# Kernel tuning notes

Measured on AMD Instinct MI355X. Metric: run time of the kernel, lower is better.

Reference implementation:

```python
import jax, jax.numpy as jnp
import numpy as np

EMBED = 2048
HEADS = 16
NOPE = 128      # embed // heads
VDIM = 128
ROPE = 64
Q_HEAD = NOPE + ROPE  # 192
KV_RANK = 512
BASE = 10000.0


def _rope(x, offset=0):
    # x: [b, h, n, d] with d even; rotary (lrpe_type=1) on pair-interleaved dims
    d = x.shape[-1]
    n = x.shape[-2]
    theta = BASE ** (-2.0 * jnp.arange(d // 2, dtype=jnp.float32) / d)  # [d/2]
    pos = jnp.arange(n, dtype=jnp.float32) + offset                     # [n]
    ang = pos[:, None] * theta[None, :]                                  # [n, d/2]
    cos, sin = jnp.cos(ang), jnp.sin(ang)
    x1 = x[..., 0::2]
    x2 = x[..., 1::2]
    o1 = x1 * cos - x2 * sin
    o2 = x1 * sin + x2 * cos
    return jnp.stack([o1, o2], axis=-1).reshape(x.shape)


def setup_inputs() -> dict:
    key = jax.random.key(0)
    ks = jax.random.split(key, 6)
    b, n = 2, 2048
    s = lambda fin: 1.0 / np.sqrt(fin)
    return {
        "x": jax.random.normal(ks[0], (b, n, EMBED), jnp.float32),
        "Wqa": jax.random.normal(ks[1], (EMBED, 512), jnp.float32) * s(EMBED),
        "Wqb": jax.random.normal(ks[2], (512, HEADS * Q_HEAD), jnp.float32) * s(512),
        "Wkva": jax.random.normal(ks[3], (EMBED, KV_RANK + ROPE), jnp.float32) * s(EMBED),
        "Wkvb": jax.random.normal(ks[4], (KV_RANK, HEADS * (NOPE + VDIM)), jnp.float32) * s(KV_RANK),
        "Wout": jax.random.normal(ks[5], (HEADS * VDIM, EMBED), jnp.float32) * s(HEADS * VDIM),
    }


def reference(x, Wqa, Wqb, Wkva, Wkvb, Wout):
    b, n, _ = x.shape
    # low-rank Q projection
    q = (x @ Wqa) @ Wqb                                   # [b, n, h*192]
    q = q.reshape(b, n, HEADS, Q_HEAD).transpose(0, 2, 1, 3)  # [b, h, n, 192]
    q_nope, q_pe = q[..., :NOPE], q[..., NOPE:]
    # low-rank KV compression + shared rope key
    ckv = x @ Wkva                                        # [b, n, 512+64]
    compressed, k_pe = ckv[..., :KV_RANK], ckv[..., KV_RANK:]
    k_pe = jnp.broadcast_to(k_pe[:, None], (b, HEADS, n, ROPE))
    kv = compressed @ Wkvb                                # [b, n, h*(128+128)]
    kv = kv.reshape(b, n, HEADS, NOPE + VDIM).transpose(0, 2, 1, 3)
    k_nope, v = kv[..., :NOPE], kv[..., NOPE:]
    # partial RoPE on rope slice
    q_pe = _rope(q_pe)
    k_pe = _rope(k_pe)
    qf = jnp.concatenate([q_nope, q_pe], axis=-1)         # [b, h, n, 192]
    kf = jnp.concatenate([k_nope, k_pe], axis=-1)
    # causal SDPA, scale = 1/sqrt(q_head_dim)
    scale = 1.0 / np.sqrt(Q_HEAD)
    scores = jnp.einsum("bhnd,bhmd->bhnm", qf, kf) * scale
    causal = jnp.tril(jnp.ones((n, n), dtype=bool))
    scores = jnp.where(causal, scores, jnp.finfo(scores.dtype).min)
    attn = jax.nn.softmax(scores, axis=-1)
    out = jnp.einsum("bhnm,bhmd->bhnd", attn, v)          # [b, h, n, 128]
    out = out.transpose(0, 2, 1, 3).reshape(b, n, HEADS * VDIM)
    return out @ Wout
```

## Files before the change

kernel.cpp:

```cpp
#include <hip/hip_runtime.h>
#include <math.h>

typedef __bf16 bf16;
typedef __bf16 bf16x8 __attribute__((ext_vector_type(8)));
typedef float f32x4 __attribute__((ext_vector_type(4)));

#define HEADS 16
#define QHEAD 192
#define NB 2
#define SEQ 2048
#define ROWS (NB * SEQ)
#define QSCALE2 0.10411754584f
#define CSHIFT 11.5415603272f
#define L2B32 0.41524101186092029f
#define INV2PI 0.15915494309189535f

__device__ __forceinline__ void rope_sincos(float n, float theta_rev,
                                            float& sn, float& cs)
{
    float rev = n * theta_rev;
    rev -= floorf(rev);
    sn = __builtin_amdgcn_sinf(rev);
    cs = __builtin_amdgcn_cosf(rev);
}

__global__ __launch_bounds__(256) void prep(
    const float* __restrict__ x,
    const float* __restrict__ Wqa, const float* __restrict__ Wqb,
    const float* __restrict__ Wkva, const float* __restrict__ Wkvb,
    const float* __restrict__ Wout,
    bf16* __restrict__ xb,
    bf16* __restrict__ WfT, bf16* __restrict__ WqbT,
    bf16* __restrict__ WkvbT, bf16* __restrict__ WoutT)
{
    int t = blockIdx.x;
    if (t < 8192) {
        size_t i = ((size_t)t * 256 + threadIdx.x) * 4;
        float4 v = *(const float4*)(x + i);
        xb[i]     = (bf16)v.x;
        xb[i + 1] = (bf16)v.y;
        xb[i + 2] = (bf16)v.z;
        xb[i + 3] = (bf16)v.w;
        return;
    }
    t -= 8192;
    __shared__ float tile[32][33];
    const float* in; bf16* out; int R, C;
    if (t < 1024)      {            in = Wqa;  out = WfT;                      R = 2048; C = 512;  }
    else if (t < 2176) { t -= 1024; in = Wkva; out = WfT + (size_t)512 * 2048; R = 2048; C = 576;  }
    else if (t < 3712) { t -= 2176; in = Wqb;  out = WqbT;                     R = 512;  C = 3072; }
    else if (t < 5760) { t -= 3712; in = Wkvb; out = WkvbT;                    R = 512;  C = 4096; }
    else               { t -= 5760; in = Wout; out = WoutT;                    R = 2048; C = 2048; }
    int tilesX = (C + 31) >> 5;
    int bx = (t % tilesX) * 32, by = (t / tilesX) * 32;
    int tx = threadIdx.x & 31, ty = threadIdx.x >> 5;
    for (int i = 0; i < 32; i += 8) {
        int r = by + ty + i, c = bx + tx;
        tile[ty + i][tx] = (r < R && c < C) ? in[(size_t)r * C + c] : 0.f;
    }
    __syncthreads();
    for (int i = 0; i < 32; i += 8) {
        int c = bx + ty + i, r = by + tx;
        if (c < C && r < R) out[(size_t)c * R + r] = (bf16)tile[tx][ty + i];
    }
}

#define GEMM_BODY(Aptr, LDA, Bptr, LDB, KK, BNIDX)                              \
    __shared__ bf16 As[128 * 32];                                               \
    __shared__ bf16 Bs[128 * 32];                                               \
    const int tid  = threadIdx.x;                                               \
    const int wave = tid >> 6, lane = tid & 63;                                 \
    const int quad = lane >> 4, l16 = lane & 15;                                \
    const int bm = blockIdx.x * 128, bn = (BNIDX) * 128;                        \
    const int wm = (wave >> 1) * 64, wn = (wave & 1) * 64;                      \
    const int srow = lane >> 2, scol = (lane & 3) * 8;                          \
    f32x4 acc[4][4];                                                            \
    for (int i = 0; i < 4; i++)                                                 \
        for (int j = 0; j < 4; j++)                                             \
            acc[i][j] = (f32x4){0.f, 0.f, 0.f, 0.f};                            \
    for (int k0 = 0; k0 < (KK); k0 += 32) {                                     \
        _Pragma("unroll")                                                       \
        for (int s2 = 0; s2 < 2; s2++) {                                        \
            const int seg = wave * 2 + s2;                                      \
            const bf16* ga = (Aptr) + (size_t)(bm + seg * 16 + srow) * (LDA) + k0 + scol; \
            const bf16* gb = (Bptr) + (size_t)(bn + seg * 16 + srow) * (LDB) + k0 + scol; \
            __builtin_amdgcn_global_load_lds(                                   \
                (const __attribute__((address_space(1))) void*)ga,              \
                (__attribute__((address_space(3))) void*)&As[seg * 512], 16, 0, 0); \
            __builtin_amdgcn_global_load_lds(                                   \
                (const __attribute__((address_space(1))) void*)gb,              \
                (__attribute__((address_space(3))) void*)&Bs[seg * 512], 16, 0, 0); \
        }                                                                       \
        __syncthreads();                                                        \
        bf16x8 af[4], bfv[4];                                                   \
        for (int mi = 0; mi < 4; mi++)                                          \
            af[mi] = *(const bf16x8*)&As[(wm + mi * 16 + l16) * 32 + quad * 8]; \
        for (int ni = 0; ni < 4; ni++)                                          \
            bfv[ni] = *(const bf16x8*)&Bs[(wn + ni * 16 + l16) * 32 + quad * 8];\
        for (int mi = 0; mi < 4; mi++)                                          \
            for (int ni = 0; ni < 4; ni++)                                      \
                acc[mi][ni] = __builtin_amdgcn_mfma_f32_16x16x32_bf16(          \
                    af[mi], bfv[ni], acc[mi][ni], 0, 0, 0);                     \
        __syncthreads();                                                        \
    }

template <typename OutT>
__global__ __launch_bounds__(256) void gemm_bf16(
    const bf16* __restrict__ A, int lda,
    const bf16* __restrict__ Bt, int ldb,
    OutT* __restrict__ C, int ldc,
    int N, int K)
{
    GEMM_BODY(A, lda, Bt, ldb, K, blockIdx.y)
    for (int mi = 0; mi < 4; mi++)
        for (int ni = 0; ni < 4; ni++) {
            int col = bn + wn + ni * 16 + l16;
            if (col >= N) continue;
            int row0 = bm + wm + mi * 16 + quad * 4;
            for (int r = 0; r < 4; r++)
                C[(size_t)(row0 + r) * ldc + col] = (OutT)acc[mi][ni][r];
        }
}

__global__ __launch_bounds__(256) void gemm_qkv(
    const bf16* __restrict__ tc,
    const bf16* __restrict__ WqbT, const bf16* __restrict__ WkvbT,
    bf16* __restrict__ qf, bf16* __restrict__ kf, bf16* __restrict__ kvv)
{
    const int byAll = blockIdx.y;
    const bool isQ = byAll < 24;
    const bf16* A  = isQ ? tc : tc + 512;
    const bf16* Bt = isQ ? WqbT : WkvbT;
    const int bnIdx = isQ ? byAll : byAll - 24;
    GEMM_BODY(A, 1152, Bt, 512, 512, bnIdx)
    if (isQ) {
        for (int mi = 0; mi < 4; mi++)
            for (int ni = 0; ni < 4; ni++) {
                int col0 = bn + wn + ni * 16;
                int h  = col0 / 192;
                int d  = col0 - h * 192 + l16;
                for (int r = 0; r < 4; r++) {
                    int row = bm + wm + mi * 16 + quad * 4 + r;
                    int b = row >> 11, n = row & 2047;
                    qf[(((size_t)(b * HEADS + h)) * SEQ + n) * QHEAD + d] =
                        (bf16)(acc[mi][ni][r] * QSCALE2);
                }
            }
    } else {
        for (int mi = 0; mi < 4; mi++)
            for (int ni = 0; ni < 4; ni++) {
                int col0 = bn + wn + ni * 16;
                int h  = col0 >> 8;
                int d0 = col0 & 255;
                int d  = d0 + l16;
                for (int r = 0; r < 4; r++) {
                    int row = bm + wm + mi * 16 + quad * 4 + r;
                    int b = row >> 11, n = row & 2047;
                    bf16 v = (bf16)acc[mi][ni][r];
                    if (d0 < 128)
                        kf[(((size_t)(b * HEADS + h)) * SEQ + n) * QHEAD + d] = v;
                    else
                        kvv[(size_t)row * 2048 + h * 128 + (d - 128)] = v;
                }
            }
    }
}

__global__ __launch_bounds__(256) void rope_vt(
    const bf16* __restrict__ tc, const bf16* __restrict__ kvv,
    bf16* __restrict__ kf, bf16* __restrict__ vT, bf16* __restrict__ qf)
{
    int t = blockIdx.x;
    if (t < 8192) {
        __shared__ bf16 tile[32][33];
        int bh = t >> 8, rest = t & 255;
        int dv0 = (rest >> 6) * 32, nt0 = (rest & 63) * 32;
        int b = bh >> 4, h = bh & 15;
        int tx = threadIdx.x & 31, ty = threadIdx.x >> 5;
        for (int i = 0; i < 32; i += 8) {
            int n = nt0 + ty + i;
            tile[ty + i][tx] = kvv[((size_t)(b * SEQ + n)) * 2048 + h * 128 + dv0 + tx];
        }
        __syncthreads();
        for (int i = 0; i < 32; i += 8) {
            int dv = dv0 + ty + i;
            vT[((size_t)bh * 128 + dv) * SEQ + nt0 + tx] = tile[tx][ty + i];
        }
    } else if (t < 9216) {
        int gid = (t - 8192) * 256 + threadIdx.x;
        int row = gid >> 6, j = gid & 63;
        int b = row >> 11, n = row & 2047;
        int i = j >> 1;
        float x1 = (float)tc[(size_t)row * 1152 + 1024 + 2 * i];
        float x2 = (float)tc[(size_t)row * 1152 + 1024 + 2 * i + 1];
        float trev = __builtin_amdgcn_exp2f(-(float)i * L2B32) * INV2PI;
        float sn, cs;
        rope_sincos((float)n, trev, sn, cs);
        bf16 rv = (bf16)((j & 1) ? (x1 * sn + x2 * cs) : (x1 * cs - x2 * sn));
        for (int h = 0; h < HEADS; h++)
            kf[(((size_t)(b * HEADS + h)) * SEQ + n) * QHEAD + 128 + j] = rv;
    } else {
        int gid = (t - 9216) * 256 + threadIdx.x;
        int base = gid * 8;
        int bh  = base >> 17;
        int rem = base & 131071;
        int n   = rem >> 6;
        int dd  = rem & 63;
        bf16* p = qf + ((size_t)bh * SEQ + n) * QHEAD + 128 + dd;
        bf16x8 v = *(const bf16x8*)p;
        bf16x8 o;
#pragma unroll
        for (int k = 0; k < 4; k++) {
            int i = (dd >> 1) + k;
            float trev = __builtin_amdgcn_exp2f(-(float)i * L2B32) * INV2PI;
            float sn, cs;
            rope_sincos((float)n, trev, sn, cs);
            float x1 = (float)v[2 * k], x2 = (float)v[2 * k + 1];
            o[2 * k]     = (bf16)(x1 * cs - x2 * sn);
            o[2 * k + 1] = (bf16)(x1 * sn + x2 * cs);
        }
        *(bf16x8*)p = o;
    }
}

__global__ __launch_bounds__(256, 2) void attn_fa(
    const bf16* __restrict__ qf, const bf16* __restrict__ kf,
    const bf16* __restrict__ vT, bf16* __restrict__ attn_out)
{
    __shared__ bf16 Ks[64][200];
    __shared__ bf16 Vt[128][72];
    __shared__ bf16 Ps[4][16][72];

    const int bid = blockIdx.x;
    const int xcd = bid & 7, j = bid >> 3;
    const int qt = 31 - (j >> 2);
    const int bh = xcd + 8 * (j & 3);
    const int b = bh >> 4, h = bh & 15;
    const int tid  = threadIdx.x;
    const int wave = tid >> 6, lane = tid & 63;
    const int quad = lane >> 4, l16 = lane & 15;

    bf16x8 aq[6];
    {
        const bf16* qbase = qf + ((size_t)bh * SEQ + qt * 64 + wave * 16 + l16) * QHEAD;
        for (int ks = 0; ks < 6; ks++)
            aq[ks] = *(const bf16x8*)(qbase + ks * 32 + quad * 8);
    }
    f32x4 o[8];
    for (int i = 0; i < 8; i++) o[i] = (f32x4){0.f, 0.f, 0.f, 0.f};
    float lp[4] = {0.f, 0.f, 0.f, 0.f};

    const bf16 *kp0, *kp1, *kp2, *kp3, *kp4, *kp5;
    bf16 *kd0, *kd1, *kd2, *kd3, *kd4, *kd5;
    const bf16 *vp0, *vp1, *vp2, *vp3;
    bf16 *vd0, *vd1, *vd2, *vd3;
#define KINIT(I)                                                                \
    { int c = tid + I * 256; int r = c / 24, col = (c - r * 24) * 8;            \
      kp##I = kf + ((size_t)bh * SEQ + r) * QHEAD + col;                        \
      kd##I = &Ks[r][col]; }
#define VINIT(I)                                                                \
    { int c = tid + I * 256; int dv = c >> 3, g = c & 7;                        \
      vp##I = vT + ((size_t)bh * 128 + dv) * SEQ + g * 8;                       \
      vd##I = &Vt[dv][g * 8]; }
    KINIT(0) KINIT(1) KINIT(2) KINIT(3) KINIT(4) KINIT(5)
    VINIT(0) VINIT(1) VINIT(2) VINIT(3)
#undef KINIT
#undef VINIT

    uint4 kb0 = *(const uint4*)kp0, kb1 = *(const uint4*)kp1,
          kb2 = *(const uint4*)kp2, kb3 = *(const uint4*)kp3,
          kb4 = *(const uint4*)kp4, kb5 = *(const uint4*)kp5;
    uint4 vb0 = *(const uint4*)vp0, vb1 = *(const uint4*)vp1,
          vb2 = *(const uint4*)vp2, vb3 = *(const uint4*)vp3;

    for (int kt = 0; kt <= qt; kt++) {
        __syncthreads();
        *(uint4*)kd0 = kb0; *(uint4*)kd1 = kb1; *(uint4*)kd2 = kb2;
        *(uint4*)kd3 = kb3; *(uint4*)kd4 = kb4; *(uint4*)kd5 = kb5;
        *(uint4*)vd0 = vb0; *(uint4*)vd1 = vb1;
        *(uint4*)vd2 = vb2; *(uint4*)vd3 = vb3;
        __syncthreads();

        if (kt < qt) {
            kp0 += 64 * QHEAD; kb0 = *(const uint4*)kp0;
            kp1 += 64 * QHEAD; kb1 = *(const uint4*)kp1;
            kp2 += 64 * QHEAD; kb2 = *(const uint4*)kp2;
            kp3 += 64 * QHEAD; kb3 = *(const uint4*)kp3;
            kp4 += 64 * QHEAD; kb4 = *(const uint4*)kp4;
            kp5 += 64 * QHEAD; kb5 = *(const uint4*)kp5;
            vp0 += 64; vb0 = *(const uint4*)vp0;
            vp1 += 64; vb1 = *(const uint4*)vp1;
            vp2 += 64; vb2 = *(const uint4*)vp2;
            vp3 += 64; vb3 = *(const uint4*)vp3;
        }

        f32x4 sacc[4];
        for (int nt = 0; nt < 4; nt++) sacc[nt] = (f32x4){0.f, 0.f, 0.f, 0.f};
        __builtin_amdgcn_s_setprio(1);
        for (int ks = 0; ks < 6; ks++)
            for (int nt = 0; nt < 4; nt++) {
                bf16x8 bk = *(const bf16x8*)&Ks[nt * 16 + l16][ks * 32 + quad * 8];
                sacc[nt] = __builtin_amdgcn_mfma_f32_16x16x32_bf16(aq[ks], bk, sacc[nt], 0, 0, 0);
            }
        __builtin_amdgcn_s_setprio(0);

        const bool diag = (kt == qt);
#pragma unroll
        for (int r = 0; r < 4; r++) {
            const int qrow = wave * 16 + quad * 4 + r;
#pragma unroll
            for (int nt = 0; nt < 4; nt++) {
                float p;
                if (diag && (nt * 16 + l16 > qrow)) p = 0.f;
                else p = __builtin_amdgcn_exp2f(sacc[nt][r] - CSHIFT);
                lp[r] += p;
                Ps[wave][quad * 4 + r][nt * 16 + l16] = (bf16)p;
            }
        }
        __builtin_amdgcn_sched_barrier(0);

        __builtin_amdgcn_s_setprio(1);
        for (int ks2 = 0; ks2 < 2; ks2++) {
            bf16x8 ap = *(const bf16x8*)&Ps[wave][l16][ks2 * 32 + quad * 8];
            for (int nv = 0; nv < 8; nv++) {
                bf16x8 bv = *(const bf16x8*)&Vt[nv * 16 + l16][ks2 * 32 + quad * 8];
                o[nv] = __builtin_amdgcn_mfma_f32_16x16x32_bf16(ap, bv, o[nv], 0, 0, 0);
            }
        }
        __builtin_amdgcn_s_setprio(0);
    }

#pragma unroll
    for (int r = 0; r < 4; r++) {
        lp[r] += __shfl_xor(lp[r], 8);
        lp[r] += __shfl_xor(lp[r], 4);
        lp[r] += __shfl_xor(lp[r], 2);
        lp[r] += __shfl_xor(lp[r], 1);
    }

    for (int r = 0; r < 4; r++) {
        float inv = 1.f / lp[r];
        size_t row = (size_t)b * SEQ + qt * 64 + wave * 16 + quad * 4 + r;
        for (int nv = 0; nv < 8; nv++)
            attn_out[row * 2048 + h * 128 + nv * 16 + l16] = (bf16)(o[nv][r] * inv);
    }
}

extern "C" void kernel_launch(void* const* d_in, const int* in_sizes, int n_in,
                              void* d_out, int out_size, void* d_ws, size_t ws_size,
                              hipStream_t stream)
{
    const float* x    = (const float*)d_in[0];
    const float* Wqa  = (const float*)d_in[1];
    const float* Wqb  = (const float*)d_in[2];
    const float* Wkva = (const float*)d_in[3];
    const float* Wkvb = (const float*)d_in[4];
    const float* Wout = (const float*)d_in[5];
    float* out = (float*)d_out;

    char* ws = (char*)d_ws;
    size_t off = 0;
    auto alloc = [&](size_t elems) { char* p = ws + off; off += elems * sizeof(bf16); return (bf16*)p; };
    bf16* xb    = alloc((size_t)ROWS * 2048);
    bf16* WfT   = alloc((size_t)1152 * 2048);
    bf16* WqbT  = alloc((size_t)3072 * 512);
    bf16* WkvbT = alloc((size_t)4096 * 512);
    bf16* WoutT = alloc((size_t)2048 * 2048);
    bf16* tc    = alloc((size_t)ROWS * 1152);
    bf16* kvv   = alloc((size_t)ROWS * 2048);
    bf16* vT    = alloc((size_t)32 * 128 * SEQ);
    bf16* qf    = alloc((size_t)32 * SEQ * QHEAD);
    bf16* kf    = alloc((size_t)32 * SEQ * QHEAD);
    bf16* attn  = xb;
    if (off > ws_size) return;

    dim3 blk(256);

    prep<<<dim3(18048), blk, 0, stream>>>(x, Wqa, Wqb, Wkva, Wkvb, Wout,
                                          xb, WfT, WqbT, WkvbT, WoutT);

    gemm_bf16<bf16><<<dim3(32, 9), blk, 0, stream>>>(xb, 2048, WfT, 2048, tc, 1152, 1088, 2048);

    gemm_qkv<<<dim3(32, 56), blk, 0, stream>>>(tc, WqbT, WkvbT, qf, kf, kvv);

    rope_vt<<<dim3(11264), blk, 0, stream>>>(tc, kvv, kf, vT, qf);

    attn_fa<<<dim3(1024), blk, 0, stream>>>(qf, kf, vT, attn);

    gemm_bf16<float><<<dim3(32, 16), blk, 0, stream>>>(attn, 2048, WoutT, 2048, out, 2048, 2048, 2048);
}
```

Baseline: 365.3 us.

## Process two 64-row query tiles per attention block to reuse K/V tiles

Each attention workgroup now handles 128 query rows (two adjacent 64-row tiles) instead of 64, so every K/V tile staged in shared memory feeds twice as many MFMAs. The grid is halved to 512 blocks. This cuts global K/V traffic and per-tile sync overhead, at the cost of doubled accumulator and Q register usage (possible spills or lower occupancy) and fewer blocks, which may hurt load balance across CUs.

New measurement: 389.4 us. 6.6% more time.

```diff
diff --git a/kernel.cpp b/kernel.cpp
--- a/kernel.cpp
+++ b/kernel.cpp
@@ -233,22 +233,29 @@
 
     const int bid = blockIdx.x;
     const int xcd = bid & 7, j = bid >> 3;
-    const int qt = 31 - (j >> 2);
+    const int qtp = 15 - (j >> 2);
     const int bh = xcd + 8 * (j & 3);
     const int b = bh >> 4, h = bh & 15;
     const int tid  = threadIdx.x;
     const int wave = tid >> 6, lane = tid & 63;
     const int quad = lane >> 4, l16 = lane & 15;
 
-    bf16x8 aq[6];
+    bf16x8 aq0[6], aq1[6];
     {
-        const bf16* qbase = qf + ((size_t)bh * SEQ + qt * 64 + wave * 16 + l16) * QHEAD;
-        for (int ks = 0; ks < 6; ks++)
-            aq[ks] = *(const bf16x8*)(qbase + ks * 32 + quad * 8);
-    }
-    f32x4 o[8];
-    for (int i = 0; i < 8; i++) o[i] = (f32x4){0.f, 0.f, 0.f, 0.f};
-    float lp[4] = {0.f, 0.f, 0.f, 0.f};
+        const bf16* qb0 = qf + ((size_t)bh * SEQ + qtp * 128 + wave * 16 + l16) * QHEAD;
+        const bf16* qb1 = qb0 + (size_t)64 * QHEAD;
+        for (int ks = 0; ks < 6; ks++) {
+            aq0[ks] = *(const bf16x8*)(qb0 + ks * 32 + quad * 8);
+            aq1[ks] = *(const bf16x8*)(qb1 + ks * 32 + quad * 8);
+        }
+    }
+    f32x4 o0[8], o1[8];
+    for (int i = 0; i < 8; i++) {
+        o0[i] = (f32x4){0.f, 0.f, 0.f, 0.f};
+        o1[i] = (f32x4){0.f, 0.f, 0.f, 0.f};
+    }
+    float lp0[4] = {0.f, 0.f, 0.f, 0.f};
+    float lp1[4] = {0.f, 0.f, 0.f, 0.f};
 
     const bf16 *kp0, *kp1, *kp2, *kp3, *kp4, *kp5;
     bf16 *kd0, *kd1, *kd2, *kd3, *kd4, *kd5;
@@ -273,7 +280,9 @@
     uint4 vb0 = *(const uint4*)vp0, vb1 = *(const uint4*)vp1,
           vb2 = *(const uint4*)vp2, vb3 = *(const uint4*)vp3;
 
-    for (int kt = 0; kt <= qt; kt++) {
+    const int ktmax = 2 * qtp + 1;
+
+    for (int kt = 0; kt <= ktmax; kt++) {
         __syncthreads();
         *(uint4*)kd0 = kb0; *(uint4*)kd1 = kb1; *(uint4*)kd2 = kb2;
         *(uint4*)kd3 = kb3; *(uint4*)kd4 = kb4; *(uint4*)kd5 = kb5;
@@ -281,7 +290,7 @@
         *(uint4*)vd2 = vb2; *(uint4*)vd3 = vb3;
         __syncthreads();
 
-        if (kt < qt) {
+        if (kt < ktmax) {
             kp0 += 64 * QHEAD; kb0 = *(const uint4*)kp0;
             kp1 += 64 * QHEAD; kb1 = *(const uint4*)kp1;
             kp2 += 64 * QHEAD; kb2 = *(const uint4*)kp2;
@@ -294,55 +303,95 @@
             vp3 += 64; vb3 = *(const uint4*)vp3;
         }
 
-        f32x4 sacc[4];
-        for (int nt = 0; nt < 4; nt++) sacc[nt] = (f32x4){0.f, 0.f, 0.f, 0.f};
+        f32x4 s0[4], s1[4];
+        for (int nt = 0; nt < 4; nt++) {
+            s0[nt] = (f32x4){0.f, 0.f, 0.f, 0.f};
+            s1[nt] = (f32x4){0.f, 0.f, 0.f, 0.f};
+        }
         __builtin_amdgcn_s_setprio(1);
         for (int ks = 0; ks < 6; ks++)
             for (int nt = 0; nt < 4; nt++) {
                 bf16x8 bk = *(const bf16x8*)&Ks[nt * 16 + l16][ks * 32 + quad * 8];
-                sacc[nt] = __builtin_amdgcn_mfma_f32_16x16x32_bf16(aq[ks], bk, sacc[nt], 0, 0, 0);
+                s0[nt] = __builtin_amdgcn_mfma_f32_16x16x32_bf16(aq0[ks], bk, s0[nt], 0, 0, 0);
+                s1[nt] = __builtin_amdgcn_mfma_f32_16x16x32_bf16(aq1[ks], bk, s1[nt], 0, 0, 0);
             }
         __builtin_amdgcn_s_setprio(0);
 
-        const bool diag = (kt == qt);
-#pragma unroll
-        for (int r = 0; r < 4; r++) {
-            const int qrow = wave * 16 + quad * 4 + r;
-#pragma unroll
-            for (int nt = 0; nt < 4; nt++) {
-                float p;
-                if (diag && (nt * 16 + l16 > qrow)) p = 0.f;
-                else p = __builtin_amdgcn_exp2f(sacc[nt][r] - CSHIFT);
-                lp[r] += p;
-                Ps[wave][quad * 4 + r][nt * 16 + l16] = (bf16)p;
-            }
-        }
-        __builtin_amdgcn_sched_barrier(0);
-
-        __builtin_amdgcn_s_setprio(1);
-        for (int ks2 = 0; ks2 < 2; ks2++) {
-            bf16x8 ap = *(const bf16x8*)&Ps[wave][l16][ks2 * 32 + quad * 8];
-            for (int nv = 0; nv < 8; nv++) {
-                bf16x8 bv = *(const bf16x8*)&Vt[nv * 16 + l16][ks2 * 32 + quad * 8];
-                o[nv] = __builtin_amdgcn_mfma_f32_16x16x32_bf16(ap, bv, o[nv], 0, 0, 0);
-            }
-        }
-        __builtin_amdgcn_s_setprio(0);
+        if (kt < ktmax) {
+            const bool diag0 = (kt == ktmax - 1);
+#pragma unroll
+            for (int r = 0; r < 4; r++) {
+                const int qrow = wave * 16 + quad * 4 + r;
+#pragma unroll
+                for (int nt = 0; nt < 4; nt++) {
+                    float p;
+                    if (diag0 && (nt * 16 + l16 > qrow)) p = 0.f;
+                    else p = __builtin_amdgcn_exp2f(s0[nt][r] - CSHIFT);
+                    lp0[r] += p;
+                    Ps[wave][quad * 4 + r][nt * 16 + l16] = (bf16)p;
+                }
+            }
+            __builtin_amdgcn_sched_barrier(0);
+            __builtin_amdgcn_s_setprio(1);
+            for (int ks2 = 0; ks2 < 2; ks2++) {
+                bf16x8 ap = *(const bf16x8*)&Ps[wave][l16][ks2 * 32 + quad * 8];
+                for (int nv = 0; nv < 8; nv++) {
+                    bf16x8 bv = *(const bf16x8*)&Vt[nv * 16 + l16][ks2 * 32 + quad * 8];
+                    o0[nv] = __builtin_amdgcn_mfma_f32_16x16x32_bf16(ap, bv, o0[nv], 0, 0, 0);
+                }
+            }
+            __builtin_amdgcn_s_setprio(0);
+            __builtin_amdgcn_sched_barrier(0);
+        }
+
+        {
+            const bool diag1 = (kt == ktmax);
+#pragma unroll
+            for (int r = 0; r < 4; r++) {
+                const int qrow = wave * 16 + quad * 4 + r;
+#pragma unroll
+                for (int nt = 0; nt < 4; nt++) {
+                    float p;
+                    if (diag1 && (nt * 16 + l16 > qrow)) p = 0.f;
+                    else p = __builtin_amdgcn_exp2f(s1[nt][r] - CSHIFT);
+                    lp1[r] += p;
+                    Ps[wave][quad * 4 + r][nt * 16 + l16] = (bf16)p;
+                }
+            }
+            __builtin_amdgcn_sched_barrier(0);
+            __builtin_amdgcn_s_setprio(1);
+            for (int ks2 = 0; ks2 < 2; ks2++) {
+                bf16x8 ap = *(const bf16x8*)&Ps[wave][l16][ks2 * 32 + quad * 8];
+                for (int nv = 0; nv < 8; nv++) {
+                    bf16x8 bv = *(const bf16x8*)&Vt[nv * 16 + l16][ks2 * 32 + quad * 8];
+                    o1[nv] = __builtin_amdgcn_mfma_f32_16x16x32_bf16(ap, bv, o1[nv], 0, 0, 0);
+                }
+            }
+            __builtin_amdgcn_s_setprio(0);
+        }
     }
 
 #pragma unroll
     for (int r = 0; r < 4; r++) {
-        lp[r] += __shfl_xor(lp[r], 8);
-        lp[r] += __shfl_xor(lp[r], 4);
-        lp[r] += __shfl_xor(lp[r], 2);
-        lp[r] += __shfl_xor(lp[r], 1);
+        lp0[r] += __shfl_xor(lp0[r], 8);
+        lp0[r] += __shfl_xor(lp0[r], 4);
+        lp0[r] += __shfl_xor(lp0[r], 2);
+        lp0[r] += __shfl_xor(lp0[r], 1);
+        lp1[r] += __shfl_xor(lp1[r], 8);
+        lp1[r] += __shfl_xor(lp1[r], 4);
+        lp1[r] += __shfl_xor(lp1[r], 2);
+        lp1[r] += __shfl_xor(lp1[r], 1);
     }
 
     for (int r = 0; r < 4; r++) {
-        float inv = 1.f / lp[r];
-        size_t row = (size_t)b * SEQ + qt * 64 + wave * 16 + quad * 4 + r;
-        for (int nv = 0; nv < 8; nv++)
-            attn_out[row * 2048 + h * 128 + nv * 16 + l16] = (bf16)(o[nv][r] * inv);
+        float inv0 = 1.f / lp0[r];
+        float inv1 = 1.f / lp1[r];
+        size_t row0 = (size_t)b * SEQ + qtp * 128 + wave * 16 + quad * 4 + r;
+        size_t row1 = row0 + 64;
+        for (int nv = 0; nv < 8; nv++) {
+            attn_out[row0 * 2048 + h * 128 + nv * 16 + l16] = (bf16)(o0[nv][r] * inv0);
+            attn_out[row1 * 2048 + h * 128 + nv * 16 + l16] = (bf16)(o1[nv][r] * inv1);
+        }
     }
 }
 
@@ -385,7 +434,7 @@
 
     rope_vt<<<dim3(11264), blk, 0, stream>>>(tc, kvv, kf, vT, qf);
 
-    attn_fa<<<dim3(1024), blk, 0, stream>>>(qf, kf, vT, attn);
+    attn_fa<<<dim3(512), blk, 0, stream>>>(qf, kf, vT, attn);
 
     gemm_bf16<float><<<dim3(32, 16), blk, 0, stream>>>(attn, 2048, WoutT, 2048, out, 2048, 2048, 2048);
 }
```
